# Kernel tuning notes

Hardware: AMD Instinct MI355X
Metric: run time of the kernel (lower is better)

## Reference

```python
import jax, jax.numpy as jnp
import numpy as np

RATE = 0.1
CLIP_MAG = 8.0
EPS = 1e-4
ACOSH_MIN = 1.0001


def _proj(v, c):
    # project_to_hyperboloid: first coord = sqrt(c + ||v[1:]||^2)
    first = jnp.sqrt(c + jnp.sum(jnp.square(v[..., 1:]), axis=-1, keepdims=True))
    return jnp.concatenate([first, v[..., 1:]], axis=-1)


def _inner_hyper(x, y):
    # Minkowski inner product: sum(x[1:]*y[1:]) - x[0]*y[0], keepdims
    p = x * y
    return jnp.sum(p[..., 1:], axis=-1, keepdims=True) - p[..., 0:1]


def _forward(vecs, curvature, mask_u):
    c = curvature  # shape [1]
    sqrt_c = jnp.sqrt(c)
    D = vecs.shape[-1]
    # origin_hyper: [sqrt(c), 0, ..., 0]
    e0 = jnp.zeros((D,), dtype=vecs.dtype).at[0].set(1.0)
    origin = e0 * sqrt_c
    o = _proj(origin, c)  # projected origin (identical to origin, kept faithful)

    # ---- logmap(vecs, origin, c) ----
    v = _proj(vecs, c)
    inner_scaled = _inner_hyper(v, o) / c  # [N,1]
    dist = sqrt_c * jnp.arccosh(jnp.maximum(-(inner_scaled + EPS), ACOSH_MIN))
    unnorm = v + o * inner_scaled
    norm_unnorm = jnp.sqrt(_inner_hyper(unnorm, unnorm))  # hyperbolic norm
    log_vecs = (dist / (norm_unnorm + EPS)) * unnorm

    # ---- dropout (training=True), keras semantics: mask & scale by 1/(1-rate) ----
    keep = (mask_u >= RATE).astype(vecs.dtype)
    dropped = log_vecs * keep / (1.0 - RATE)

    # ---- expmap(dropped, origin, c) ----
    snv = jnp.linalg.norm(dropped, axis=-1, keepdims=True) / sqrt_c + EPS
    snv_c = jnp.clip(snv, -CLIP_MAG, CLIP_MAG)
    return jnp.cosh(snv_c) * o + (jnp.sinh(snv_c) / snv) * dropped


def setup_inputs() -> dict:
    key = jax.random.key(0)
    k1, k2 = jax.random.split(key)
    N, D = 16384, 512
    vecs = jax.random.normal(k1, (N, D), dtype=jnp.float32)
    curvature = jnp.ones((1,), dtype=jnp.float32)
    mask_u = jax.random.uniform(k2, (N, D), dtype=jnp.float32)
    return {"vecs": vecs, "curvature": curvature, "mask_u": mask_u}


def reference(vecs, curvature, mask_u):
    return _forward(vecs, curvature, mask_u)
```

## Files before the change

kernel.cpp:

```cpp
#include <hip/hip_runtime.h>
#include <math.h>

#define RATE 0.1f
#define INV_KEEP (1.0f / 0.9f)
#define EPS 1e-4f
#define CLIP_MAG 8.0f
#define ACOSH_MIN 1.0001f

__global__ __launch_bounds__(256) void hyp_dropout_kernel(
    const float* __restrict__ vecs,
    const float* __restrict__ curv,
    const float* __restrict__ mask,
    float* __restrict__ out,
    int nrows)
{
    const int wave = blockIdx.x * 4 + (threadIdx.x >> 6);
    const int lane = threadIdx.x & 63;
    if (wave >= nrows) return;

    const size_t base = (size_t)wave * 512;
    const float4* vr = (const float4*)(vecs + base);
    const float4* mr = (const float4*)(mask + base);

    float4 va = vr[lane];
    float4 vb = vr[lane + 64];
    float4 ma = mr[lane];
    float4 mb = mr[lane + 64];

    const float ka0 = (ma.x >= RATE) ? 1.f : 0.f;
    const float ka1 = (ma.y >= RATE) ? 1.f : 0.f;
    const float ka2 = (ma.z >= RATE) ? 1.f : 0.f;
    const float ka3 = (ma.w >= RATE) ? 1.f : 0.f;
    const float kb0 = (mb.x >= RATE) ? 1.f : 0.f;
    const float kb1 = (mb.y >= RATE) ? 1.f : 0.f;
    const float kb2 = (mb.z >= RATE) ? 1.f : 0.f;
    const float kb3 = (mb.w >= RATE) ? 1.f : 0.f;

    const float a0 = (lane == 0) ? 0.f : va.x;

    float s2 = a0 * a0;
    float m2 = ka0 * a0 * a0;
    s2 = fmaf(va.y, va.y, s2); m2 = fmaf(ka1 * va.y, va.y, m2);
    s2 = fmaf(va.z, va.z, s2); m2 = fmaf(ka2 * va.z, va.z, m2);
    s2 = fmaf(va.w, va.w, s2); m2 = fmaf(ka3 * va.w, va.w, m2);
    s2 = fmaf(vb.x, vb.x, s2); m2 = fmaf(kb0 * vb.x, vb.x, m2);
    s2 = fmaf(vb.y, vb.y, s2); m2 = fmaf(kb1 * vb.y, vb.y, m2);
    s2 = fmaf(vb.z, vb.z, s2); m2 = fmaf(kb2 * vb.z, vb.z, m2);
    s2 = fmaf(vb.w, vb.w, s2); m2 = fmaf(kb3 * vb.w, vb.w, m2);

    #pragma unroll
    for (int off = 32; off > 0; off >>= 1) {
        s2 += __shfl_xor(s2, off, 64);
        m2 += __shfl_xor(m2, off, 64);
    }

    const float c = curv[0];
    const float sqrt_c = sqrtf(c);

    const float v0 = sqrtf(c + s2);
    const float arg = fmaxf(v0 / sqrt_c - EPS, ACOSH_MIN);
    const float dist = sqrt_c * acoshf(arg);
    const float scale1 = dist / (sqrtf(s2) + EPS);
    const float k = scale1 * INV_KEEP;

    const float sn = k * sqrtf(m2);
    const float snv = sn / sqrt_c + EPS;
    const float snv_c = fminf(fmaxf(snv, -CLIP_MAG), CLIP_MAG);
    const float sh = sinhf(snv_c) / snv;
    const float ch = coshf(snv_c) * sqrt_c;

    const float w = sh * k;
    float4 oa, ob;
    oa.x = (lane == 0) ? ch : w * ka0 * va.x;
    oa.y = w * ka1 * va.y;
    oa.z = w * ka2 * va.z;
    oa.w = w * ka3 * va.w;
    ob.x = w * kb0 * vb.x;
    ob.y = w * kb1 * vb.y;
    ob.z = w * kb2 * vb.z;
    ob.w = w * kb3 * vb.w;

    float4* orow = (float4*)(out + base);
    orow[lane] = oa;
    orow[lane + 64] = ob;
}

extern "C" void kernel_launch(void* const* d_in, const int* in_sizes, int n_in,
                              void* d_out, int out_size, void* d_ws, size_t ws_size,
                              hipStream_t stream) {
    const float* vecs = (const float*)d_in[0];
    const float* curv = (const float*)d_in[1];
    const float* mask = (const float*)d_in[2];
    float* out = (float*)d_out;

    const int nrows = in_sizes[0] / 512;
    const int waves_per_block = 4;
    const int grid = (nrows + waves_per_block - 1) / waves_per_block;

    hyp_dropout_kernel<<<grid, 256, 0, stream>>>(vecs, curv, mask, out, nrows);
}
```

Measured before the change: 101.2 us.

## Use nontemporal loads/stores, fast intrinsics for acosh/sinh/cosh, and select-based masking

```diff
diff --git a/kernel.cpp b/kernel.cpp
--- a/kernel.cpp
+++ b/kernel.cpp
@@ -6,6 +6,18 @@
 #define EPS 1e-4f
 #define CLIP_MAG 8.0f
 #define ACOSH_MIN 1.0001f
+
+typedef float floatx4 __attribute__((ext_vector_type(4)));
+
+__device__ __forceinline__ float fast_exp(float x) {
+    return __builtin_amdgcn_exp2f(x * 1.44269504088896341f);
+}
+__device__ __forceinline__ float fast_log(float x) {
+    return __builtin_amdgcn_logf(x) * 0.69314718055994531f;
+}
+__device__ __forceinline__ float fast_rcp(float x) {
+    return __builtin_amdgcn_rcpf(x);
+}
 
 __global__ __launch_bounds__(256) void hyp_dropout_kernel(
     const float* __restrict__ vecs,
@@ -19,34 +31,34 @@
     if (wave >= nrows) return;
 
     const size_t base = (size_t)wave * 512;
-    const float4* vr = (const float4*)(vecs + base);
-    const float4* mr = (const float4*)(mask + base);
+    const floatx4* vr = (const floatx4*)(vecs + base);
+    const floatx4* mr = (const floatx4*)(mask + base);
 
-    float4 va = vr[lane];
-    float4 vb = vr[lane + 64];
-    float4 ma = mr[lane];
-    float4 mb = mr[lane + 64];
-
-    const float ka0 = (ma.x >= RATE) ? 1.f : 0.f;
-    const float ka1 = (ma.y >= RATE) ? 1.f : 0.f;
-    const float ka2 = (ma.z >= RATE) ? 1.f : 0.f;
-    const float ka3 = (ma.w >= RATE) ? 1.f : 0.f;
-    const float kb0 = (mb.x >= RATE) ? 1.f : 0.f;
-    const float kb1 = (mb.y >= RATE) ? 1.f : 0.f;
-    const float kb2 = (mb.z >= RATE) ? 1.f : 0.f;
-    const float kb3 = (mb.w >= RATE) ? 1.f : 0.f;
+    const floatx4 va = __builtin_nontemporal_load(&vr[lane]);
+    const floatx4 vb = __builtin_nontemporal_load(&vr[lane + 64]);
+    const floatx4 ma = __builtin_nontemporal_load(&mr[lane]);
+    const floatx4 mb = __builtin_nontemporal_load(&mr[lane + 64]);
 
     const float a0 = (lane == 0) ? 0.f : va.x;
 
+    const float xa0 = (ma.x >= RATE) ? a0   : 0.f;
+    const float xa1 = (ma.y >= RATE) ? va.y : 0.f;
+    const float xa2 = (ma.z >= RATE) ? va.z : 0.f;
+    const float xa3 = (ma.w >= RATE) ? va.w : 0.f;
+    const float xb0 = (mb.x >= RATE) ? vb.x : 0.f;
+    const float xb1 = (mb.y >= RATE) ? vb.y : 0.f;
+    const float xb2 = (mb.z >= RATE) ? vb.z : 0.f;
+    const float xb3 = (mb.w >= RATE) ? vb.w : 0.f;
+
     float s2 = a0 * a0;
-    float m2 = ka0 * a0 * a0;
-    s2 = fmaf(va.y, va.y, s2); m2 = fmaf(ka1 * va.y, va.y, m2);
-    s2 = fmaf(va.z, va.z, s2); m2 = fmaf(ka2 * va.z, va.z, m2);
-    s2 = fmaf(va.w, va.w, s2); m2 = fmaf(ka3 * va.w, va.w, m2);
-    s2 = fmaf(vb.x, vb.x, s2); m2 = fmaf(kb0 * vb.x, vb.x, m2);
-    s2 = fmaf(vb.y, vb.y, s2); m2 = fmaf(kb1 * vb.y, vb.y, m2);
-    s2 = fmaf(vb.z, vb.z, s2); m2 = fmaf(kb2 * vb.z, vb.z, m2);
-    s2 = fmaf(vb.w, vb.w, s2); m2 = fmaf(kb3 * vb.w, vb.w, m2);
+    float m2 = xa0 * xa0;
+    s2 = fmaf(va.y, va.y, s2); m2 = fmaf(xa1, xa1, m2);
+    s2 = fmaf(va.z, va.z, s2); m2 = fmaf(xa2, xa2, m2);
+    s2 = fmaf(va.w, va.w, s2); m2 = fmaf(xa3, xa3, m2);
+    s2 = fmaf(vb.x, vb.x, s2); m2 = fmaf(xb0, xb0, m2);
+    s2 = fmaf(vb.y, vb.y, s2); m2 = fmaf(xb1, xb1, m2);
+    s2 = fmaf(vb.z, vb.z, s2); m2 = fmaf(xb2, xb2, m2);
+    s2 = fmaf(vb.w, vb.w, s2); m2 = fmaf(xb3, xb3, m2);
 
     #pragma unroll
     for (int off = 32; off > 0; off >>= 1) {
@@ -56,33 +68,35 @@
 
     const float c = curv[0];
     const float sqrt_c = sqrtf(c);
+    const float rc = fast_rcp(sqrt_c);
 
     const float v0 = sqrtf(c + s2);
-    const float arg = fmaxf(v0 / sqrt_c - EPS, ACOSH_MIN);
-    const float dist = sqrt_c * acoshf(arg);
-    const float scale1 = dist / (sqrtf(s2) + EPS);
-    const float k = scale1 * INV_KEEP;
+    const float arg = fmaxf(fmaf(v0, rc, -EPS), ACOSH_MIN);
+    const float acosh_arg = fast_log(arg + sqrtf(fmaf(arg, arg, -1.f)));
+    const float dist = sqrt_c * acosh_arg;
+    const float k = dist * fast_rcp(sqrtf(s2) + EPS) * INV_KEEP;
 
-    const float sn = k * sqrtf(m2);
-    const float snv = sn / sqrt_c + EPS;
+    const float snv = fmaf(k * sqrtf(m2), rc, EPS);
     const float snv_c = fminf(fmaxf(snv, -CLIP_MAG), CLIP_MAG);
-    const float sh = sinhf(snv_c) / snv;
-    const float ch = coshf(snv_c) * sqrt_c;
+    const float e  = fast_exp(snv_c);
+    const float ei = fast_rcp(e);
+    const float sh = 0.5f * (e - ei) * fast_rcp(snv);
+    const float ch = 0.5f * (e + ei) * sqrt_c;
 
     const float w = sh * k;
-    float4 oa, ob;
-    oa.x = (lane == 0) ? ch : w * ka0 * va.x;
-    oa.y = w * ka1 * va.y;
-    oa.z = w * ka2 * va.z;
-    oa.w = w * ka3 * va.w;
-    ob.x = w * kb0 * vb.x;
-    ob.y = w * kb1 * vb.y;
-    ob.z = w * kb2 * vb.z;
-    ob.w = w * kb3 * vb.w;
+    floatx4 oa, ob;
+    oa.x = (lane == 0) ? ch : w * xa0;
+    oa.y = w * xa1;
+    oa.z = w * xa2;
+    oa.w = w * xa3;
+    ob.x = w * xb0;
+    ob.y = w * xb1;
+    ob.z = w * xb2;
+    ob.w = w * xb3;
 
-    float4* orow = (float4*)(out + base);
-    orow[lane] = oa;
-    orow[lane + 64] = ob;
+    floatx4* orow = (floatx4*)(out + base);
+    __builtin_nontemporal_store(oa, &orow[lane]);
+    __builtin_nontemporal_store(ob, &orow[lane + 64]);
 }
 
 extern "C" void kernel_launch(void* const* d_in, const int* in_sizes, int n_in,
```

Measured after the change: 109.0 us. +7.7%, slower.
